# Optimization experiments

Measured on AMD Instinct MI355X. Metric: run time of the kernel, lower is better.

The kernel has to match this reference:

```python
import jax, jax.numpy as jnp
import numpy as np
import math

D_K = 64
DROP_P = 0.5

def setup_inputs() -> dict:
    key = jax.random.key(0)
    kq, kk, kv, km = jax.random.split(key, 4)
    B, S, d = 32, 2048, D_K
    Q = jax.random.normal(kq, (B, S, d), dtype=jnp.float32)
    K = jax.random.normal(kk, (B, S, d), dtype=jnp.float32)
    V = jax.random.normal(kv, (B, S, d), dtype=jnp.float32)
    # Bernoulli(keep_prob) mask for training-mode dropout (p=0.5)
    dropout_mask = jax.random.bernoulli(km, 1.0 - DROP_P, (B, S, S))
    return {"Q": Q, "K": K, "V": V, "dropout_mask": dropout_mask}

def reference(Q, K, V, dropout_mask):
    # attn = softmax(Q K^T / sqrt(d_k)); dropout; y = attn V
    scale = 1.0 / math.sqrt(D_K)
    scores = jnp.einsum('bqd,bkd->bqk', Q, K) * scale   # [B,S,S]
    attn = jax.nn.softmax(scores, axis=-1)
    keep_scale = 1.0 / (1.0 - DROP_P)
    attn = jnp.where(dropout_mask, attn * keep_scale, 0.0)
    y = jnp.einsum('bqk,bkd->bqd', attn, V)             # [B,S,d]
    return (y, attn)
```

## Files before the change

kernel.cpp:

```cpp
#include <hip/hip_runtime.h>
#include <hip/hip_bf16.h>
#include <stdint.h>

#define SQ 2048
#define DK 64
#define NB 32
#define TQ 16
#define EW 2064
#define NTHREADS 512
#define SCL 0.18033688011112042f

typedef __attribute__((ext_vector_type(8))) short short8;
typedef __attribute__((ext_vector_type(4))) float f32x4;
typedef __attribute__((ext_vector_type(4))) unsigned u32x4;
typedef __attribute__((ext_vector_type(2))) unsigned u32x2;

__device__ __forceinline__ unsigned f2bf_u(float x) {
    unsigned u = __builtin_bit_cast(unsigned, x);
    u += 0x7fffu + ((u >> 16) & 1u);
    return u >> 16;
}
__device__ __forceinline__ float bf2f(unsigned h) {
    return __builtin_bit_cast(float, h << 16);
}
__device__ __forceinline__ float bf2f_hi(unsigned u) {
    return __builtin_bit_cast(float, u & 0xffff0000u);
}
__device__ __forceinline__ void split8(const float* p, short8& h, short8& l) {
    f32x4 a = *(const f32x4*)p;
    f32x4 b = *(const f32x4*)(p + 4);
    #pragma unroll
    for (int j = 0; j < 4; ++j) {
        unsigned ua = f2bf_u(a[j]);
        h[j] = (short)ua; l[j] = (short)f2bf_u(a[j] - bf2f(ua));
        unsigned ub = f2bf_u(b[j]);
        h[j + 4] = (short)ub; l[j + 4] = (short)f2bf_u(b[j] - bf2f(ub));
    }
}

__global__ __launch_bounds__(256) void prep_kernel(
    const float* __restrict__ K, const float* __restrict__ V,
    unsigned short* __restrict__ Khi, unsigned short* __restrict__ Klo,
    unsigned short* __restrict__ Vt)
{
    __shared__ float vtile[64][65];
    const int t  = threadIdx.x;
    const int b  = blockIdx.x >> 5;
    const int s0 = (blockIdx.x & 31) << 6;
    const size_t base = ((size_t)b * SQ + s0) * DK + (size_t)t * 16;

    {
        short8 h0, l0, h1, l1;
        split8(K + base,     h0, l0);
        split8(K + base + 8, h1, l1);
        *(short8*)(Khi + base)     = h0;
        *(short8*)(Khi + base + 8) = h1;
        *(short8*)(Klo + base)     = l0;
        *(short8*)(Klo + base + 8) = l1;
    }
    {
        const int sr = t >> 2, dc = (t & 3) << 4;
        #pragma unroll
        for (int u = 0; u < 16; u += 4) {
            f32x4 v = *(const f32x4*)(V + base + u);
            vtile[sr][dc + u + 0] = v[0];
            vtile[sr][dc + u + 1] = v[1];
            vtile[sr][dc + u + 2] = v[2];
            vtile[sr][dc + u + 3] = v[3];
        }
    }
    __syncthreads();
    #pragma unroll
    for (int rep = 0; rep < 16; ++rep) {
        const int idx = rep * 256 + t;
        const int d = idx >> 6, s = idx & 63;
        Vt[((size_t)b * DK + d) * SQ + s0 + s] = (unsigned short)f2bf_u(vtile[s][d]);
    }
}

__global__ __launch_bounds__(NTHREADS, 4) void sdpa_main(
    const float* __restrict__ Q, const unsigned short* __restrict__ Khi,
    const unsigned short* __restrict__ Klo, const unsigned short* __restrict__ Vt,
    const unsigned* __restrict__ Mk, float* __restrict__ Yout, float* __restrict__ Aout)
{
    __shared__ __align__(16) unsigned short e_lds[TQ][EW];
    __shared__ float yp[4][TQ][16];
    __shared__ float rsum[8][TQ];
    __shared__ float i2s[TQ];

    const int tid  = threadIdx.x;
    const int lane = tid & 63;
    const int wv   = tid >> 6;
    const int m16  = lane & 15;
    const int kq   = lane >> 4;
    const int koff = kq * 8;

    const int b  = blockIdx.x >> 7;
    const int q0 = (blockIdx.x & 127) * TQ;

    short8 qh[2], ql[2];
    {
        const float* qrow = Q + ((size_t)b * SQ + q0 + m16) * DK;
        split8(qrow + koff,      qh[0], ql[0]);
        split8(qrow + 32 + koff, qh[1], ql[1]);
    }

    float rs = 0.f;
    {
        const size_t krow = ((size_t)b * SQ + wv * 256 + m16) * DK;
        const unsigned short* khp = Khi + krow;
        const unsigned short* klp = Klo + krow;
        const unsigned* mrow = Mk + ((size_t)b * SQ + q0 + m16) * SQ + wv * 256 + kq * 4;
        const int xw = (m16 & 7) << 3;

        u32x4 m0, m1, m2, m3, m4, m5, m6, m7;

        #define LOADM(dst, t) dst = *(const u32x4*)(mrow + (t) * 16);
        #define AITER(t, M)                                                           \
        {                                                                             \
            const int off = (t) * 16 * DK;                                            \
            f32x4 acc = {0.f, 0.f, 0.f, 0.f};                                         \
            _Pragma("unroll")                                                         \
            for (int c = 0; c < 2; ++c) {                                             \
                short8 kh = *(const short8*)(khp + off + c * 32 + koff);              \
                short8 kl = *(const short8*)(klp + off + c * 32 + koff);              \
                acc = __builtin_amdgcn_mfma_f32_16x16x32_bf16(kh, qh[c], acc, 0, 0, 0);\
                acc = __builtin_amdgcn_mfma_f32_16x16x32_bf16(kh, ql[c], acc, 0, 0, 0);\
                acc = __builtin_amdgcn_mfma_f32_16x16x32_bf16(kl, qh[c], acc, 0, 0, 0);\
            }                                                                         \
            const float e0 = exp2f(acc[0] * SCL);                                     \
            const float e1 = exp2f(acc[1] * SCL);                                     \
            const float e2 = exp2f(acc[2] * SCL);                                     \
            const float e3 = exp2f(acc[3] * SCL);                                     \
            rs += (e0 + e1) + (e2 + e3);                                              \
            const float a0 = (M)[0] ? e0 : 0.f;                                       \
            const float a1 = (M)[1] ? e1 : 0.f;                                       \
            const float a2 = (M)[2] ? e2 : 0.f;                                       \
            const float a3 = (M)[3] ? e3 : 0.f;                                       \
            u32x2 pk;                                                                 \
            pk[0] = f2bf_u(a0) | (f2bf_u(a1) << 16);                                  \
            pk[1] = f2bf_u(a2) | (f2bf_u(a3) << 16);                                  \
            *(u32x2*)&e_lds[m16][(wv * 256 + (t) * 16 + kq * 4) ^ xw] = pk;           \
        }

        LOADM(m0, 0)  LOADM(m1, 1)  LOADM(m2, 2)  LOADM(m3, 3)
        LOADM(m4, 4)  LOADM(m5, 5)  LOADM(m6, 6)  LOADM(m7, 7)
        AITER(0, m0)  AITER(1, m1)  AITER(2, m2)  AITER(3, m3)
        LOADM(m0, 8)  LOADM(m1, 9)  LOADM(m2, 10) LOADM(m3, 11)
        AITER(4, m4)  AITER(5, m5)  AITER(6, m6)  AITER(7, m7)
        LOADM(m4, 12) LOADM(m5, 13) LOADM(m6, 14) LOADM(m7, 15)
        AITER(8, m0)  AITER(9, m1)  AITER(10, m2) AITER(11, m3)
        AITER(12, m4) AITER(13, m5) AITER(14, m6) AITER(15, m7)

        #undef AITER
        #undef LOADM
    }
    rs += __shfl_xor(rs, 16);
    rs += __shfl_xor(rs, 32);
    if (lane < 16) rsum[wv][lane] = rs;
    __syncthreads();
    if (tid < 16) {
        float s = 0.f;
        #pragma unroll
        for (int w = 0; w < 8; ++w) s += rsum[w][tid];
        i2s[tid] = 2.0f / s;
    }
    __syncthreads();

    const int cr = tid >> 5;
    const int cc = (tid & 31) * 8;
    const int xc = (cr & 7) << 3;
    const float i2 = i2s[cr];
    const size_t crow = ((size_t)b * SQ + q0 + cr) * SQ + cc;

    const int g   = wv >> 1;
    const int par = wv & 1;
    const int xm  = (m16 & 7) << 3;
    const unsigned short* vrow = Vt + ((size_t)b * DK + g * 16 + m16) * SQ;
    f32x4 acc = {0.f, 0.f, 0.f, 0.f};

    #define CSTRIPE(s)                                                            \
    {                                                                             \
        const u32x4 ev = *(const u32x4*)&e_lds[cr][((s) * 256 + cc) ^ xc];        \
        f32x4 o0, o1;                                                             \
        o0[0] = bf2f(ev[0] & 0xffffu) * i2;  o0[1] = bf2f_hi(ev[0]) * i2;         \
        o0[2] = bf2f(ev[1] & 0xffffu) * i2;  o0[3] = bf2f_hi(ev[1]) * i2;         \
        o1[0] = bf2f(ev[2] & 0xffffu) * i2;  o1[1] = bf2f_hi(ev[2]) * i2;         \
        o1[2] = bf2f(ev[3] & 0xffffu) * i2;  o1[3] = bf2f_hi(ev[3]) * i2;         \
        __builtin_nontemporal_store(o0, (f32x4*)(Aout + crow + (s) * 256));       \
        __builtin_nontemporal_store(o1, (f32x4*)(Aout + crow + (s) * 256 + 4));   \
    }
    #define PVSTRIPE(s)                                                           \
    {                                                                             \
        _Pragma("unroll")                                                         \
        for (int c = 0; c < 4; ++c) {                                             \
            const int k0 = (s) * 256 + par * 128 + c * 32;                        \
            short8 af = *(const short8*)&e_lds[m16][(k0 + koff) ^ xm];            \
            short8 vf = *(const short8*)(vrow + k0 + koff);                       \
            acc = __builtin_amdgcn_mfma_f32_16x16x32_bf16(af, vf, acc, 0, 0, 0);  \
        }                                                                         \
    }

    CSTRIPE(0) PVSTRIPE(0)
    CSTRIPE(1) PVSTRIPE(1)
    CSTRIPE(2) PVSTRIPE(2)
    CSTRIPE(3) PVSTRIPE(3)
    CSTRIPE(4) PVSTRIPE(4)
    CSTRIPE(5) PVSTRIPE(5)
    CSTRIPE(6) PVSTRIPE(6)
    CSTRIPE(7) PVSTRIPE(7)

    #undef PVSTRIPE
    #undef CSTRIPE

    if (par == 1) {
        #pragma unroll
        for (int r = 0; r < 4; ++r) yp[g][kq * 4 + r][m16] = acc[r];
    }
    __syncthreads();
    if (par == 0) {
        #pragma unroll
        for (int r = 0; r < 4; ++r) {
            const float yv = (acc[r] + yp[g][kq * 4 + r][m16]) * i2s[kq * 4 + r];
            __builtin_nontemporal_store(yv,
                Yout + ((size_t)b * SQ + q0 + kq * 4 + r) * DK + g * 16 + m16);
        }
    }
}

extern "C" void kernel_launch(void* const* d_in, const int* in_sizes, int n_in,
                              void* d_out, int out_size, void* d_ws, size_t ws_size,
                              hipStream_t stream) {
    const float*    Q  = (const float*)d_in[0];
    const float*    K  = (const float*)d_in[1];
    const float*    V  = (const float*)d_in[2];
    const unsigned* Mk = (const unsigned*)d_in[3];
    float* Yout = (float*)d_out;
    float* Aout = (float*)d_out + (size_t)NB * SQ * DK;

    const size_t NEL = (size_t)NB * SQ * DK;
    unsigned short* Khi = (unsigned short*)d_ws;
    unsigned short* Klo = Khi + NEL;
    unsigned short* Vt  = Klo + NEL;

    prep_kernel<<<dim3(NB * (SQ / 64)), dim3(256), 0, stream>>>(K, V, Khi, Klo, Vt);
    sdpa_main<<<dim3(NB * (SQ / TQ)), dim3(NTHREADS), 0, stream>>>(
        Q, Khi, Klo, Vt, Mk, Yout, Aout);
}
```

Measured before the change: 512.0 us.

## Software-pipeline K, mask and V loads; remap blocks to XCDs by batch

Result: slower. 523.9 us (+2.3%).

```diff
diff --git a/kernel.cpp b/kernel.cpp
--- a/kernel.cpp
+++ b/kernel.cpp
@@ -95,8 +95,11 @@
     const int kq   = lane >> 4;
     const int koff = kq * 8;
 
-    const int b  = blockIdx.x >> 7;
-    const int q0 = (blockIdx.x & 127) * TQ;
+    const int bx = blockIdx.x;
+    const int xcd = bx & 7;
+    const int j   = bx >> 3;
+    const int b   = xcd * 4 + (j >> 7);
+    const int q0  = (j & 127) * TQ;
 
     short8 qh[2], ql[2];
     {
@@ -113,47 +116,66 @@
         const unsigned* mrow = Mk + ((size_t)b * SQ + q0 + m16) * SQ + wv * 256 + kq * 4;
         const int xw = (m16 & 7) << 3;
 
-        u32x4 m0, m1, m2, m3, m4, m5, m6, m7;
-
-        #define LOADM(dst, t) dst = *(const u32x4*)(mrow + (t) * 16);
-        #define AITER(t, M)                                                           \
-        {                                                                             \
-            const int off = (t) * 16 * DK;                                            \
-            f32x4 acc = {0.f, 0.f, 0.f, 0.f};                                         \
-            _Pragma("unroll")                                                         \
-            for (int c = 0; c < 2; ++c) {                                             \
-                short8 kh = *(const short8*)(khp + off + c * 32 + koff);              \
-                short8 kl = *(const short8*)(klp + off + c * 32 + koff);              \
-                acc = __builtin_amdgcn_mfma_f32_16x16x32_bf16(kh, qh[c], acc, 0, 0, 0);\
-                acc = __builtin_amdgcn_mfma_f32_16x16x32_bf16(kh, ql[c], acc, 0, 0, 0);\
-                acc = __builtin_amdgcn_mfma_f32_16x16x32_bf16(kl, qh[c], acc, 0, 0, 0);\
-            }                                                                         \
-            const float e0 = exp2f(acc[0] * SCL);                                     \
-            const float e1 = exp2f(acc[1] * SCL);                                     \
-            const float e2 = exp2f(acc[2] * SCL);                                     \
-            const float e3 = exp2f(acc[3] * SCL);                                     \
-            rs += (e0 + e1) + (e2 + e3);                                              \
-            const float a0 = (M)[0] ? e0 : 0.f;                                       \
-            const float a1 = (M)[1] ? e1 : 0.f;                                       \
-            const float a2 = (M)[2] ? e2 : 0.f;                                       \
-            const float a3 = (M)[3] ? e3 : 0.f;                                       \
-            u32x2 pk;                                                                 \
-            pk[0] = f2bf_u(a0) | (f2bf_u(a1) << 16);                                  \
-            pk[1] = f2bf_u(a2) | (f2bf_u(a3) << 16);                                  \
-            *(u32x2*)&e_lds[m16][(wv * 256 + (t) * 16 + kq * 4) ^ xw] = pk;           \
-        }
-
-        LOADM(m0, 0)  LOADM(m1, 1)  LOADM(m2, 2)  LOADM(m3, 3)
-        LOADM(m4, 4)  LOADM(m5, 5)  LOADM(m6, 6)  LOADM(m7, 7)
-        AITER(0, m0)  AITER(1, m1)  AITER(2, m2)  AITER(3, m3)
-        LOADM(m0, 8)  LOADM(m1, 9)  LOADM(m2, 10) LOADM(m3, 11)
-        AITER(4, m4)  AITER(5, m5)  AITER(6, m6)  AITER(7, m7)
-        LOADM(m4, 12) LOADM(m5, 13) LOADM(m6, 14) LOADM(m7, 15)
-        AITER(8, m0)  AITER(9, m1)  AITER(10, m2) AITER(11, m3)
-        AITER(12, m4) AITER(13, m5) AITER(14, m6) AITER(15, m7)
+        #define KDEF(t) short8 kh0_##t, kh1_##t, kl0_##t, kl1_##t;
+        #define KLOAD(t) {                                                        \
+            const int off = (t) * 16 * DK;                                        \
+            kh0_##t = *(const short8*)(khp + off + koff);                         \
+            kh1_##t = *(const short8*)(khp + off + 32 + koff);                    \
+            kl0_##t = *(const short8*)(klp + off + koff);                         \
+            kl1_##t = *(const short8*)(klp + off + 32 + koff); }
+        #define MDEF(t) u32x4 m_##t;
+        #define MLOAD(t) m_##t = __builtin_nontemporal_load((const u32x4*)(mrow + (t) * 16));
+        #define AITER(t) {                                                        \
+            f32x4 acc = {0.f, 0.f, 0.f, 0.f};                                     \
+            acc = __builtin_amdgcn_mfma_f32_16x16x32_bf16(kh0_##t, qh[0], acc, 0, 0, 0); \
+            acc = __builtin_amdgcn_mfma_f32_16x16x32_bf16(kh0_##t, ql[0], acc, 0, 0, 0); \
+            acc = __builtin_amdgcn_mfma_f32_16x16x32_bf16(kl0_##t, qh[0], acc, 0, 0, 0); \
+            acc = __builtin_amdgcn_mfma_f32_16x16x32_bf16(kh1_##t, qh[1], acc, 0, 0, 0); \
+            acc = __builtin_amdgcn_mfma_f32_16x16x32_bf16(kh1_##t, ql[1], acc, 0, 0, 0); \
+            acc = __builtin_amdgcn_mfma_f32_16x16x32_bf16(kl1_##t, qh[1], acc, 0, 0, 0); \
+            const float e0 = __builtin_amdgcn_exp2f(acc[0] * SCL);                \
+            const float e1 = __builtin_amdgcn_exp2f(acc[1] * SCL);                \
+            const float e2 = __builtin_amdgcn_exp2f(acc[2] * SCL);                \
+            const float e3 = __builtin_amdgcn_exp2f(acc[3] * SCL);                \
+            rs += (e0 + e1) + (e2 + e3);                                          \
+            const float a0 = m_##t[0] ? e0 : 0.f;                                 \
+            const float a1 = m_##t[1] ? e1 : 0.f;                                 \
+            const float a2 = m_##t[2] ? e2 : 0.f;                                 \
+            const float a3 = m_##t[3] ? e3 : 0.f;                                 \
+            u32x2 pk;                                                             \
+            pk[0] = f2bf_u(a0) | (f2bf_u(a1) << 16);                              \
+            pk[1] = f2bf_u(a2) | (f2bf_u(a3) << 16);                              \
+            *(u32x2*)&e_lds[m16][(wv * 256 + (t) * 16 + kq * 4) ^ xw] = pk; }
+
+        KDEF(0)  KDEF(1)  KDEF(2)  KDEF(3)  KDEF(4)  KDEF(5)  KDEF(6)  KDEF(7)
+        KDEF(8)  KDEF(9)  KDEF(10) KDEF(11) KDEF(12) KDEF(13) KDEF(14) KDEF(15)
+        MDEF(0)  MDEF(1)  MDEF(2)  MDEF(3)  MDEF(4)  MDEF(5)  MDEF(6)  MDEF(7)
+        MDEF(8)  MDEF(9)  MDEF(10) MDEF(11) MDEF(12) MDEF(13) MDEF(14) MDEF(15)
+
+        KLOAD(0)  KLOAD(1)
+        MLOAD(0)  MLOAD(1)  MLOAD(2)  MLOAD(3)
+        KLOAD(2)  MLOAD(4)   AITER(0)
+        KLOAD(3)  MLOAD(5)   AITER(1)
+        KLOAD(4)  MLOAD(6)   AITER(2)
+        KLOAD(5)  MLOAD(7)   AITER(3)
+        KLOAD(6)  MLOAD(8)   AITER(4)
+        KLOAD(7)  MLOAD(9)   AITER(5)
+        KLOAD(8)  MLOAD(10)  AITER(6)
+        KLOAD(9)  MLOAD(11)  AITER(7)
+        KLOAD(10) MLOAD(12)  AITER(8)
+        KLOAD(11) MLOAD(13)  AITER(9)
+        KLOAD(12) MLOAD(14)  AITER(10)
+        KLOAD(13) MLOAD(15)  AITER(11)
+        KLOAD(14)            AITER(12)
+        KLOAD(15)            AITER(13)
+                             AITER(14)
+                             AITER(15)
 
         #undef AITER
-        #undef LOADM
+        #undef MLOAD
+        #undef MDEF
+        #undef KLOAD
+        #undef KDEF
     }
     rs += __shfl_xor(rs, 16);
     rs += __shfl_xor(rs, 32);
@@ -173,9 +195,9 @@
     const float i2 = i2s[cr];
     const size_t crow = ((size_t)b * SQ + q0 + cr) * SQ + cc;
 
-    const int g   = wv >> 1;
-    const int par = wv & 1;
-    const int xm  = (m16 & 7) << 3;
+    const int g    = wv >> 1;
+    const int parh = (wv & 1) * 128;
+    const int xm   = (m16 & 7) << 3;
     const unsigned short* vrow = Vt + ((size_t)b * DK + g * 16 + m16) * SQ;
     f32x4 acc = {0.f, 0.f, 0.f, 0.f};
 
@@ -190,35 +212,47 @@
         __builtin_nontemporal_store(o0, (f32x4*)(Aout + crow + (s) * 256));       \
         __builtin_nontemporal_store(o1, (f32x4*)(Aout + crow + (s) * 256 + 4));   \
     }
-    #define PVSTRIPE(s)                                                           \
-    {                                                                             \
-        _Pragma("unroll")                                                         \
-        for (int c = 0; c < 4; ++c) {                                             \
-            const int k0 = (s) * 256 + par * 128 + c * 32;                        \
-            short8 af = *(const short8*)&e_lds[m16][(k0 + koff) ^ xm];            \
-            short8 vf = *(const short8*)(vrow + k0 + koff);                       \
-            acc = __builtin_amdgcn_mfma_f32_16x16x32_bf16(af, vf, acc, 0, 0, 0);  \
-        }                                                                         \
-    }
-
-    CSTRIPE(0) PVSTRIPE(0)
-    CSTRIPE(1) PVSTRIPE(1)
-    CSTRIPE(2) PVSTRIPE(2)
-    CSTRIPE(3) PVSTRIPE(3)
-    CSTRIPE(4) PVSTRIPE(4)
-    CSTRIPE(5) PVSTRIPE(5)
-    CSTRIPE(6) PVSTRIPE(6)
-    CSTRIPE(7) PVSTRIPE(7)
-
-    #undef PVSTRIPE
+    #define VDEF(u) short8 vf_##u;
+    #define VLOAD(u) vf_##u = *(const short8*)(vrow + ((u) >> 2) * 256 + parh + ((u) & 3) * 32 + koff);
+    #define PV1(u) {                                                              \
+        const int k0 = ((u) >> 2) * 256 + parh + ((u) & 3) * 32;                  \
+        short8 af = *(const short8*)&e_lds[m16][(k0 + koff) ^ xm];                \
+        acc = __builtin_amdgcn_mfma_f32_16x16x32_bf16(af, vf_##u, acc, 0, 0, 0); }
+
+    VDEF(0)  VDEF(1)  VDEF(2)  VDEF(3)  VDEF(4)  VDEF(5)  VDEF(6)  VDEF(7)
+    VDEF(8)  VDEF(9)  VDEF(10) VDEF(11) VDEF(12) VDEF(13) VDEF(14) VDEF(15)
+    VDEF(16) VDEF(17) VDEF(18) VDEF(19) VDEF(20) VDEF(21) VDEF(22) VDEF(23)
+    VDEF(24) VDEF(25) VDEF(26) VDEF(27) VDEF(28) VDEF(29) VDEF(30) VDEF(31)
+
+    VLOAD(0) VLOAD(1) VLOAD(2) VLOAD(3)
+    CSTRIPE(0)
+    PV1(0)  VLOAD(4)  PV1(1)  VLOAD(5)  PV1(2)  VLOAD(6)  PV1(3)  VLOAD(7)
+    CSTRIPE(1)
+    PV1(4)  VLOAD(8)  PV1(5)  VLOAD(9)  PV1(6)  VLOAD(10) PV1(7)  VLOAD(11)
+    CSTRIPE(2)
+    PV1(8)  VLOAD(12) PV1(9)  VLOAD(13) PV1(10) VLOAD(14) PV1(11) VLOAD(15)
+    CSTRIPE(3)
+    PV1(12) VLOAD(16) PV1(13) VLOAD(17) PV1(14) VLOAD(18) PV1(15) VLOAD(19)
+    CSTRIPE(4)
+    PV1(16) VLOAD(20) PV1(17) VLOAD(21) PV1(18) VLOAD(22) PV1(19) VLOAD(23)
+    CSTRIPE(5)
+    PV1(20) VLOAD(24) PV1(21) VLOAD(25) PV1(22) VLOAD(26) PV1(23) VLOAD(27)
+    CSTRIPE(6)
+    PV1(24) VLOAD(28) PV1(25) VLOAD(29) PV1(26) VLOAD(30) PV1(27) VLOAD(31)
+    CSTRIPE(7)
+    PV1(28) PV1(29) PV1(30) PV1(31)
+
+    #undef PV1
+    #undef VLOAD
+    #undef VDEF
     #undef CSTRIPE
 
-    if (par == 1) {
+    if ((wv & 1) == 1) {
         #pragma unroll
         for (int r = 0; r < 4; ++r) yp[g][kq * 4 + r][m16] = acc[r];
     }
     __syncthreads();
-    if (par == 0) {
+    if ((wv & 1) == 0) {
         #pragma unroll
         for (int r = 0; r < 4; ++r) {
             const float yv = (acc[r] + yp[g][kq * 4 + r][m16]) * i2s[kq * 4 + r];
```
